# Kernel tuning notes

Hardware: AMD Instinct MI355X
Metric: run time of the kernel (lower is better)

Reference implementation:

```python
import math
import jax, jax.numpy as jnp
import numpy as np

B, A, T, C, H, WF = 8, 64, 128, 256, 8, 4
EPS = 1e-5


def setup_inputs() -> dict:
    key = jax.random.key(0)
    ks = jax.random.split(key, 16)
    s = 0.02
    inp = {
        "x": jax.random.normal(ks[0], (B, A, T, C), dtype=jnp.float32),
        "mask_x": jax.random.bernoulli(ks[1], 0.1, (B, A, T)),
        "ln1_w": jnp.ones((C,), jnp.float32),
        "ln1_b": jnp.zeros((C,), jnp.float32),
        "qkv_w": jax.random.normal(ks[2], (3 * C, C), jnp.float32) * s,
        "qkv_b": jnp.zeros((3 * C,), jnp.float32),
        "proj_w": jax.random.normal(ks[3], (C, C), jnp.float32) * s,
        "proj_b": jnp.zeros((C,), jnp.float32),
        "ln2_w": jnp.ones((C,), jnp.float32),
        "ln2_b": jnp.zeros((C,), jnp.float32),
        "fc1_w": jax.random.normal(ks[4], (WF * C, C), jnp.float32) * s,
        "fc1_b": jnp.zeros((WF * C,), jnp.float32),
        "fc2_w": jax.random.normal(ks[5], (C, WF * C), jnp.float32) * s,
        "fc2_b": jnp.zeros((C,), jnp.float32),
    }
    return inp


def _layer_norm(v, w, b):
    m = jnp.mean(v, axis=-1, keepdims=True)
    var = jnp.var(v, axis=-1, keepdims=True)
    return (v - m) * jax.lax.rsqrt(var + EPS) * w + b


def reference(x, mask_x, ln1_w, ln1_b, qkv_w, qkv_b, proj_w, proj_b,
              ln2_w, ln2_b, fc1_w, fc1_b, fc2_w, fc2_b):
    b, a, t, c = x.shape
    h = H
    d = c // h
    # x = ln_1(x); residual is taken AFTER ln_1, matching the torch code
    x1 = _layer_norm(x, ln1_w, ln1_b)
    qkv = x1 @ qkv_w.T + qkv_b  # (B,A,T,3C)
    q, k, v = jnp.split(qkv, 3, axis=-1)
    q = q.reshape(b, a, t, h, d)
    k = k.reshape(b, a, t, h, d)
    v = v.reshape(b, a, t, h, d)
    # attention across time, per agent: (B,A,H,T,T)
    att = jnp.einsum('bathd,bashd->bahts', q, k) * (1.0 / math.sqrt(d))
    mask_val = -jnp.finfo(jnp.float32).max
    # mask broadcast over query rows (torch repeats mask over key dim too,
    # but the pattern masks entire query rows t)
    att = jnp.where(mask_x[:, :, None, :, None], mask_val, att)
    att = jax.nn.softmax(att, axis=-1)
    y = jnp.einsum('bahts,bashd->bathd', att, v).reshape(b, a, t, c)
    y = y @ proj_w.T + proj_b
    x2 = x1 + y
    x3 = _layer_norm(x2, ln2_w, ln2_b)
    mlp = jax.nn.gelu(x3 @ fc1_w.T + fc1_b, approximate=False) @ fc2_w.T + fc2_b
    return x3 + mlp
```

## Files before the change

kernel.cpp:

```cpp
#include <hip/hip_runtime.h>
#include <hip/hip_bf16.h>

typedef unsigned short u16;
typedef unsigned int   u32;

static constexpr int Bc = 8, Ac = 64, Tc = 128, Cc = 256, Hc = 8;
static constexpr int NROW = Bc * Ac * Tc;
static constexpr int DH = Cc / Hc;

__device__ __forceinline__ float bf2f(u16 h) {
    u32 u = ((u32)h) << 16; float f; __builtin_memcpy(&f, &u, 4); return f;
}
__device__ __forceinline__ u16 f2bf(float f) {
    u32 u; __builtin_memcpy(&u, &f, 4);
    u += 0x7fffu + ((u >> 16) & 1u);
    return (u16)(u >> 16);
}

typedef __attribute__((ext_vector_type(8))) short  short8v;
typedef __attribute__((ext_vector_type(4))) float  float4v;

__device__ __forceinline__ void gload16(const void* g, const void* lds) {
    __builtin_amdgcn_global_load_lds(
        (const __attribute__((address_space(1))) void*)g,
        (__attribute__((address_space(3))) void*)lds, 16, 0, 0);
}

#define MFMA16(a, b, c) __builtin_amdgcn_mfma_f32_16x16x32_bf16((a), (b), (c), 0, 0, 0)

__global__ void cast4_kernel(const float* __restrict__ a, int na,
                             const float* __restrict__ b, int nb,
                             const float* __restrict__ c, int nc,
                             const float* __restrict__ d, int nd,
                             u16* oa, u16* ob, u16* oc, u16* od) {
    int i = blockIdx.x * 256 + threadIdx.x;
    if (i < na) { oa[i] = f2bf(a[i]); return; }
    i -= na;
    if (i < nb) { ob[i] = f2bf(b[i]); return; }
    i -= nb;
    if (i < nc) { oc[i] = f2bf(c[i]); return; }
    i -= nc;
    if (i < nd) { od[i] = f2bf(d[i]); }
}

__global__ __launch_bounds__(256) void ln_f32(const float* __restrict__ in,
        const float* __restrict__ w, const float* __restrict__ b,
        u16* __restrict__ out) {
    int row  = blockIdx.x * 4 + (threadIdx.x >> 6);
    int lane = threadIdx.x & 63;
    const float* rp = in + (size_t)row * Cc + lane * 4;
    float4 v = *(const float4*)rp;
    float s  = v.x + v.y + v.z + v.w;
    float sq = v.x * v.x + v.y * v.y + v.z * v.z + v.w * v.w;
    for (int off = 32; off; off >>= 1) { s += __shfl_xor(s, off); sq += __shfl_xor(sq, off); }
    float mean = s * (1.f / Cc);
    float rs = rsqrtf(sq * (1.f / Cc) - mean * mean + 1e-5f);
    int c0 = lane * 4;
    float vv[4] = {v.x, v.y, v.z, v.w};
    ushort4 ov;
    ov.x = f2bf((vv[0] - mean) * rs * w[c0 + 0] + b[c0 + 0]);
    ov.y = f2bf((vv[1] - mean) * rs * w[c0 + 1] + b[c0 + 1]);
    ov.z = f2bf((vv[2] - mean) * rs * w[c0 + 2] + b[c0 + 2]);
    ov.w = f2bf((vv[3] - mean) * rs * w[c0 + 3] + b[c0 + 3]);
    *(ushort4*)(out + (size_t)row * Cc + c0) = ov;
}

__global__ __launch_bounds__(256) void ln_bf16(const u16* __restrict__ in,
        const float* __restrict__ w, const float* __restrict__ b,
        u16* __restrict__ out) {
    int row  = blockIdx.x * 4 + (threadIdx.x >> 6);
    int lane = threadIdx.x & 63;
    const u16* rp = in + (size_t)row * Cc + lane * 4;
    ushort4 hv = *(const ushort4*)rp;
    float vv[4] = {bf2f(hv.x), bf2f(hv.y), bf2f(hv.z), bf2f(hv.w)};
    float s = vv[0] + vv[1] + vv[2] + vv[3];
    float sq = vv[0]*vv[0] + vv[1]*vv[1] + vv[2]*vv[2] + vv[3]*vv[3];
    for (int off = 32; off; off >>= 1) { s += __shfl_xor(s, off); sq += __shfl_xor(sq, off); }
    float mean = s * (1.f / Cc);
    float rs = rsqrtf(sq * (1.f / Cc) - mean * mean + 1e-5f);
    int c0 = lane * 4;
    ushort4 ov;
    ov.x = f2bf((vv[0] - mean) * rs * w[c0 + 0] + b[c0 + 0]);
    ov.y = f2bf((vv[1] - mean) * rs * w[c0 + 1] + b[c0 + 1]);
    ov.z = f2bf((vv[2] - mean) * rs * w[c0 + 2] + b[c0 + 2]);
    ov.w = f2bf((vv[3] - mean) * rs * w[c0 + 3] + b[c0 + 3]);
    *(ushort4*)(out + (size_t)row * Cc + c0) = ov;
}

template<int K, int EPI>
__global__ __launch_bounds__(256) void gemm128p(
        const u16* __restrict__ X, const u16* __restrict__ W,
        const float* __restrict__ bias,
        u16* __restrict__ outb, float* __restrict__ outf,
        const u16* __restrict__ res, int Nf, int nbn) {
    constexpr int NK = K / 32;
    __shared__ __align__(16) u16 lA[3][128][32];
    __shared__ __align__(16) u16 lB[3][128][32];
    const int nwg = gridDim.x;
    const int q8  = nwg >> 3;
    const int lid = (blockIdx.x & 7) * q8 + (blockIdx.x >> 3);
    const int bn  = (lid % nbn) * 128;
    const int bm  = (lid / nbn) * 128;
    const int tid = threadIdx.x, lane = tid & 63, wave = tid >> 6;
    const int wr = (wave >> 1) * 64, wc = (wave & 1) * 64;
    const int lr = lane & 15, lg = lane >> 4;

    auto stage = [&](int k0, int buf) {
        #pragma unroll
        for (int qq = 0; qq < 2; qq++) {
            const int cbase = wave * 128 + qq * 64;
            const int c   = cbase + lane;
            const int row = c >> 2, p = c & 3;
            const int gc  = p ^ ((row >> 1) & 3);
            gload16(X + (size_t)(bm + row) * K + k0 + gc * 8,
                    (const u16*)&lA[buf][0][0] + (size_t)cbase * 8);
            gload16(W + (size_t)(bn + row) * K + k0 + gc * 8,
                    (const u16*)&lB[buf][0][0] + (size_t)cbase * 8);
        }
    };

    stage(0, 0);
    stage(32, 1);

    const int rchunk = (lg ^ ((lr >> 1) & 3)) * 8;

    float4v acc[4][4] = {};
    for (int k = 0; k < NK; ++k) {
        if (k + 1 < NK) asm volatile("s_waitcnt vmcnt(4)" ::: "memory");
        else            asm volatile("s_waitcnt vmcnt(0)" ::: "memory");
        __builtin_amdgcn_s_barrier();
        if (k + 2 < NK) stage((k + 2) * 32, (k + 2) % 3);
        const int cur = k % 3;
        short8v a[4], b[4];
        #pragma unroll
        for (int i = 0; i < 4; i++) a[i] = *(const short8v*)&lB[cur][wc + i * 16 + lr][rchunk];
        #pragma unroll
        for (int j = 0; j < 4; j++) b[j] = *(const short8v*)&lA[cur][wr + j * 16 + lr][rchunk];
        #pragma unroll
        for (int i = 0; i < 4; i++)
            #pragma unroll
            for (int j = 0; j < 4; j++)
                acc[i][j] = MFMA16(a[i], b[j], acc[i][j]);
    }

    #pragma unroll
    for (int i = 0; i < 4; i++) {
        const int n0 = bn + wc + i * 16 + lg * 4;
        const float4 bv = *(const float4*)&bias[n0];
        #pragma unroll
        for (int j = 0; j < 4; j++) {
            const int m = bm + wr + j * 16 + lr;
            const size_t o0 = (size_t)m * Nf + n0;
            float v0 = acc[i][j][0] + bv.x;
            float v1 = acc[i][j][1] + bv.y;
            float v2 = acc[i][j][2] + bv.z;
            float v3 = acc[i][j][3] + bv.w;
            if (EPI == 1 || EPI == 3) {
                ushort4 rv = *(const ushort4*)(res + o0);
                v0 += bf2f(rv.x); v1 += bf2f(rv.y); v2 += bf2f(rv.z); v3 += bf2f(rv.w);
            }
            if (EPI == 2) {
                v0 = 0.5f * v0 * (1.f + erff(v0 * 0.70710678118654752f));
                v1 = 0.5f * v1 * (1.f + erff(v1 * 0.70710678118654752f));
                v2 = 0.5f * v2 * (1.f + erff(v2 * 0.70710678118654752f));
                v3 = 0.5f * v3 * (1.f + erff(v3 * 0.70710678118654752f));
            }
            if (EPI == 3) {
                float4 o; o.x = v0; o.y = v1; o.z = v2; o.w = v3;
                *(float4*)(outf + o0) = o;
            } else {
                ushort4 o;
                o.x = f2bf(v0); o.y = f2bf(v1); o.z = f2bf(v2); o.w = f2bf(v3);
                *(ushort4*)(outb + o0) = o;
            }
        }
    }
}

__global__ __launch_bounds__(256) void attn_mfma(
        const u16* __restrict__ qkv, const unsigned char* __restrict__ mask,
        u16* __restrict__ out) {
    __shared__ u16 sk[128][32];
    __shared__ u16 svt[32][136];
    __shared__ u16 sp[4][32][136];
    __shared__ unsigned char smask[128];
    const int ba = blockIdx.x;
    const size_t rowbase = (size_t)ba * Tc;
    const int tid  = threadIdx.x;
    const int lane = tid & 63;
    const int wave = tid >> 6;
    const int wq0  = wave * 32;
    const int lrow = lane & 15, lg = lane >> 4;
    if (tid < 128) smask[tid] = mask[rowbase + tid];

    const float scale  = 0.17677669529663687f;
    const float inv128 = 1.0f / 128.0f;
    const float4v zero4 = {0.f, 0.f, 0.f, 0.f};

    for (int h = 0; h < Hc; h++) {
        {
            const int r = tid >> 1, half = tid & 1;
            const u16* gbase = qkv + (rowbase + r) * 768 + h * 32 + half * 16;
            uint4 k0 = *(const uint4*)(gbase + 256);
            uint4 k1 = *(const uint4*)(gbase + 256 + 8);
            *(uint4*)&sk[r][half * 16]     = k0;
            *(uint4*)&sk[r][half * 16 + 8] = k1;
            uint4 v0 = *(const uint4*)(gbase + 512);
            uint4 v1 = *(const uint4*)(gbase + 512 + 8);
            u16 vt[16];
            *(uint4*)&vt[0] = v0; *(uint4*)&vt[8] = v1;
            #pragma unroll
            for (int e = 0; e < 16; e++) svt[half * 16 + e][r] = vt[e];
        }
        __syncthreads();

        short8v a0, a1;
        {
            const u16* qp0 = qkv + (rowbase + wq0 + lrow) * 768 + h * 32 + lg * 8;
            const u16* qp1 = qp0 + 16 * 768;
            a0 = *(const short8v*)qp0;
            a1 = *(const short8v*)qp1;
        }
        float4v s_acc[2][8];
        #pragma unroll
        for (int j = 0; j < 8; j++) {
            short8v bj = *(const short8v*)&sk[j * 16 + lrow][lg * 8];
            s_acc[0][j] = MFMA16(a0, bj, zero4);
            s_acc[1][j] = MFMA16(a1, bj, zero4);
        }

        #pragma unroll
        for (int i = 0; i < 2; i++) {
            #pragma unroll
            for (int r = 0; r < 4; r++) {
                float m = s_acc[i][0][r];
                #pragma unroll
                for (int j = 1; j < 8; j++) m = fmaxf(m, s_acc[i][j][r]);
                #pragma unroll
                for (int off = 1; off < 16; off <<= 1) m = fmaxf(m, __shfl_xor(m, off));
                float sum = 0.f;
                #pragma unroll
                for (int j = 0; j < 8; j++) {
                    float e = __expf((s_acc[i][j][r] - m) * scale);
                    sum += e;
                    s_acc[i][j][r] = e;
                }
                #pragma unroll
                for (int off = 1; off < 16; off <<= 1) sum += __shfl_xor(sum, off);
                const int qloc = i * 16 + lg * 4 + r;
                const bool mk = smask[wq0 + qloc] != 0;
                const float invs = 1.f / sum;
                #pragma unroll
                for (int j = 0; j < 8; j++) {
                    float pv = mk ? inv128 : s_acc[i][j][r] * invs;
                    sp[wave][qloc][j * 16 + lrow] = f2bf(pv);
                }
            }
        }

        float4v o_acc[2][2] = {};
        #pragma unroll
        for (int t = 0; t < 4; t++) {
            short8v pa0 = *(const short8v*)&sp[wave][lrow][t * 32 + lg * 8];
            short8v pa1 = *(const short8v*)&sp[wave][16 + lrow][t * 32 + lg * 8];
            short8v vb0 = *(const short8v*)&svt[lrow][t * 32 + lg * 8];
            short8v vb1 = *(const short8v*)&svt[16 + lrow][t * 32 + lg * 8];
            o_acc[0][0] = MFMA16(pa0, vb0, o_acc[0][0]);
            o_acc[0][1] = MFMA16(pa0, vb1, o_acc[0][1]);
            o_acc[1][0] = MFMA16(pa1, vb0, o_acc[1][0]);
            o_acc[1][1] = MFMA16(pa1, vb1, o_acc[1][1]);
        }

        #pragma unroll
        for (int i = 0; i < 2; i++)
            #pragma unroll
            for (int n = 0; n < 2; n++)
                #pragma unroll
                for (int r = 0; r < 4; r++) {
                    size_t row = rowbase + wq0 + i * 16 + lg * 4 + r;
                    int col = h * 32 + n * 16 + lrow;
                    out[row * 256 + col] = f2bf(o_acc[i][n][r]);
                }
        __syncthreads();
    }
}

extern "C" void kernel_launch(void* const* d_in, const int* in_sizes, int n_in,
                              void* d_out, int out_size, void* d_ws, size_t ws_size,
                              hipStream_t stream) {
    const float* x      = (const float*)d_in[0];
    const unsigned char* mask = (const unsigned char*)d_in[1];
    const float* ln1_w  = (const float*)d_in[2];
    const float* ln1_b  = (const float*)d_in[3];
    const float* qkv_w  = (const float*)d_in[4];
    const float* qkv_b  = (const float*)d_in[5];
    const float* proj_w = (const float*)d_in[6];
    const float* proj_b = (const float*)d_in[7];
    const float* ln2_w  = (const float*)d_in[8];
    const float* ln2_b  = (const float*)d_in[9];
    const float* fc1_w  = (const float*)d_in[10];
    const float* fc1_b  = (const float*)d_in[11];
    const float* fc2_w  = (const float*)d_in[12];
    const float* fc2_b  = (const float*)d_in[13];
    float* out = (float*)d_out;

    char* ws = (char*)d_ws;
    size_t off = 0;
    auto alloc = [&](size_t elems) -> u16* {
        u16* p = (u16*)(ws + off);
        off += ((elems * 2 + 255) / 256) * 256;
        return p;
    };
    u16* wqb  = alloc(768 * 256);
    u16* wpb  = alloc(256 * 256);
    u16* w1b  = alloc(1024 * 256);
    u16* w2b  = alloc(256 * 1024);
    u16* x1b  = alloc((size_t)NROW * Cc);
    u16* qkvb = alloc((size_t)NROW * 3 * Cc);
    u16* attb = alloc((size_t)NROW * Cc);
    u16* x2b  = alloc((size_t)NROW * Cc);
    u16* hb   = qkvb;
    u16* x3b  = x1b;

    cast4_kernel<<<(786432 + 255) / 256, 256, 0, stream>>>(
        qkv_w, 196608, proj_w, 65536, fc1_w, 262144, fc2_w, 262144,
        wqb, wpb, w1b, w2b);
    ln_f32<<<NROW / 4, 256, 0, stream>>>(x, ln1_w, ln1_b, x1b);
    gemm128p<256, 0><<<512 * 6, 256, 0, stream>>>(
        x1b, wqb, qkv_b, qkvb, nullptr, nullptr, 768, 6);
    attn_mfma<<<Bc * Ac, 256, 0, stream>>>(qkvb, mask, attb);
    gemm128p<256, 1><<<512 * 2, 256, 0, stream>>>(
        attb, wpb, proj_b, x2b, nullptr, x1b, 256, 2);
    ln_bf16<<<NROW / 4, 256, 0, stream>>>(x2b, ln2_w, ln2_b, x3b);
    gemm128p<256, 2><<<512 * 8, 256, 0, stream>>>(
        x3b, w1b, fc1_b, hb, nullptr, nullptr, 1024, 8);
    gemm128p<1024, 3><<<512 * 2, 256, 0, stream>>>(
        hb, w2b, fc2_b, nullptr, out, x3b, 256, 2);
}
```

Before: 333.7 us.

## Stage bf16 GEMM epilogue through LDS for coalesced stores; use tanh GELU

For the bf16-output GEMM epilogues, results are first written to a padded LDS tile, which reuses the input staging buffers, and then written to global memory as coalesced 16-byte rows instead of scattered 8-byte stores. The exact erf GELU is replaced by a tanh approximation built on __expf to cut transcendental cost. This adds two barriers and an LDS round trip. The tanh GELU is an approximation of the reference's exact GELU and may add small numeric error.

```diff
diff --git a/kernel.cpp b/kernel.cpp
--- a/kernel.cpp
+++ b/kernel.cpp
@@ -15,6 +15,14 @@
     u32 u; __builtin_memcpy(&u, &f, 4);
     u += 0x7fffu + ((u >> 16) & 1u);
     return (u16)(u >> 16);
+}
+
+__device__ __forceinline__ float gelu_f(float x) {
+    float y = 0.7978845608028654f * (x + 0.044715f * x * x * x);
+    float t = __expf(-2.0f * fabsf(y));
+    float th = (1.0f - t) / (1.0f + t);
+    th = copysignf(th, y);
+    return 0.5f * x * (1.0f + th);
 }
 
 typedef __attribute__((ext_vector_type(8))) short  short8v;
@@ -94,8 +102,9 @@
         u16* __restrict__ outb, float* __restrict__ outf,
         const u16* __restrict__ res, int Nf, int nbn) {
     constexpr int NK = K / 32;
-    __shared__ __align__(16) u16 lA[3][128][32];
-    __shared__ __align__(16) u16 lB[3][128][32];
+    __shared__ __align__(16) u16 smem[24576];
+    u16* lA = smem;
+    u16* lB = smem + 12288;
     const int nwg = gridDim.x;
     const int q8  = nwg >> 3;
     const int lid = (blockIdx.x & 7) * q8 + (blockIdx.x >> 3);
@@ -113,9 +122,9 @@
             const int row = c >> 2, p = c & 3;
             const int gc  = p ^ ((row >> 1) & 3);
             gload16(X + (size_t)(bm + row) * K + k0 + gc * 8,
-                    (const u16*)&lA[buf][0][0] + (size_t)cbase * 8);
+                    lA + (size_t)buf * 4096 + (size_t)cbase * 8);
             gload16(W + (size_t)(bn + row) * K + k0 + gc * 8,
-                    (const u16*)&lB[buf][0][0] + (size_t)cbase * 8);
+                    lB + (size_t)buf * 4096 + (size_t)cbase * 8);
         }
     };
 
@@ -133,9 +142,11 @@
         const int cur = k % 3;
         short8v a[4], b[4];
         #pragma unroll
-        for (int i = 0; i < 4; i++) a[i] = *(const short8v*)&lB[cur][wc + i * 16 + lr][rchunk];
-        #pragma unroll
-        for (int j = 0; j < 4; j++) b[j] = *(const short8v*)&lA[cur][wr + j * 16 + lr][rchunk];
+        for (int i = 0; i < 4; i++)
+            a[i] = *(const short8v*)&lB[cur * 4096 + (wc + i * 16 + lr) * 32 + rchunk];
+        #pragma unroll
+        for (int j = 0; j < 4; j++)
+            b[j] = *(const short8v*)&lA[cur * 4096 + (wr + j * 16 + lr) * 32 + rchunk];
         #pragma unroll
         for (int i = 0; i < 4; i++)
             #pragma unroll
@@ -143,36 +154,58 @@
                 acc[i][j] = MFMA16(a[i], b[j], acc[i][j]);
     }
 
-    #pragma unroll
-    for (int i = 0; i < 4; i++) {
-        const int n0 = bn + wc + i * 16 + lg * 4;
-        const float4 bv = *(const float4*)&bias[n0];
-        #pragma unroll
-        for (int j = 0; j < 4; j++) {
-            const int m = bm + wr + j * 16 + lr;
-            const size_t o0 = (size_t)m * Nf + n0;
-            float v0 = acc[i][j][0] + bv.x;
-            float v1 = acc[i][j][1] + bv.y;
-            float v2 = acc[i][j][2] + bv.z;
-            float v3 = acc[i][j][3] + bv.w;
-            if (EPI == 1 || EPI == 3) {
+    if (EPI == 3) {
+        #pragma unroll
+        for (int i = 0; i < 4; i++) {
+            const int n0 = bn + wc + i * 16 + lg * 4;
+            const float4 bv = *(const float4*)&bias[n0];
+            #pragma unroll
+            for (int j = 0; j < 4; j++) {
+                const int m = bm + wr + j * 16 + lr;
+                const size_t o0 = (size_t)m * Nf + n0;
                 ushort4 rv = *(const ushort4*)(res + o0);
-                v0 += bf2f(rv.x); v1 += bf2f(rv.y); v2 += bf2f(rv.z); v3 += bf2f(rv.w);
+                float4 o;
+                o.x = acc[i][j][0] + bv.x + bf2f(rv.x);
+                o.y = acc[i][j][1] + bv.y + bf2f(rv.y);
+                o.z = acc[i][j][2] + bv.z + bf2f(rv.z);
+                o.w = acc[i][j][3] + bv.w + bf2f(rv.w);
+                *(float4*)(outf + o0) = o;
             }
-            if (EPI == 2) {
-                v0 = 0.5f * v0 * (1.f + erff(v0 * 0.70710678118654752f));
-                v1 = 0.5f * v1 * (1.f + erff(v1 * 0.70710678118654752f));
-                v2 = 0.5f * v2 * (1.f + erff(v2 * 0.70710678118654752f));
-                v3 = 0.5f * v3 * (1.f + erff(v3 * 0.70710678118654752f));
-            }
-            if (EPI == 3) {
-                float4 o; o.x = v0; o.y = v1; o.z = v2; o.w = v3;
-                *(float4*)(outf + o0) = o;
-            } else {
+        }
+    } else {
+        __syncthreads();
+        u16* ot = smem;
+        #pragma unroll
+        for (int i = 0; i < 4; i++) {
+            const int n0l = wc + i * 16 + lg * 4;
+            const float4 bv = *(const float4*)&bias[bn + n0l];
+            #pragma unroll
+            for (int j = 0; j < 4; j++) {
+                const int ml = wr + j * 16 + lr;
+                float v0 = acc[i][j][0] + bv.x;
+                float v1 = acc[i][j][1] + bv.y;
+                float v2 = acc[i][j][2] + bv.z;
+                float v3 = acc[i][j][3] + bv.w;
+                if (EPI == 1) {
+                    const size_t o0 = (size_t)(bm + ml) * Nf + bn + n0l;
+                    ushort4 rv = *(const ushort4*)(res + o0);
+                    v0 += bf2f(rv.x); v1 += bf2f(rv.y); v2 += bf2f(rv.z); v3 += bf2f(rv.w);
+                }
+                if (EPI == 2) {
+                    v0 = gelu_f(v0); v1 = gelu_f(v1); v2 = gelu_f(v2); v3 = gelu_f(v3);
+                }
                 ushort4 o;
                 o.x = f2bf(v0); o.y = f2bf(v1); o.z = f2bf(v2); o.w = f2bf(v3);
-                *(ushort4*)(outb + o0) = o;
+                *(ushort4*)&ot[ml * 136 + n0l] = o;
             }
+        }
+        __syncthreads();
+        #pragma unroll
+        for (int i2 = 0; i2 < 8; i2++) {
+            const int c   = i2 * 256 + tid;
+            const int row = c >> 4, ch = c & 15;
+            *(uint4*)(outb + (size_t)(bm + row) * Nf + bn + ch * 8) =
+                *(const uint4*)&ot[row * 136 + ch * 8];
         }
     }
 }
```

Measured after the change: 313.8 us. 5.9% less time.
